# Kernel optimization log

Hardware: AMD Instinct MI355X
Metric: run time of the kernel (lower is better)

The kernel has to match this reference:

```python
import jax, jax.numpy as jnp
import numpy as np

D_IN, D_K, D_V = 1024, 128, 128
B, S = 8, 4096


def setup_inputs() -> dict:
    key = jax.random.key(0)
    kq, kk, kv, kwq, kwk, kwv = jax.random.split(key, 6)
    q = jax.random.normal(kq, (B, S, D_IN), dtype=jnp.float32)
    k = jax.random.normal(kk, (B, S, D_IN), dtype=jnp.float32)
    v = jax.random.normal(kv, (B, S, D_IN), dtype=jnp.float32)
    # nn.Linear(d_in, d_out, bias=None): weight shape [d_out, d_in], y = x @ W^T
    scale = 1.0 / np.sqrt(D_IN)
    Wq = jax.random.uniform(kwq, (D_K, D_IN), jnp.float32, -scale, scale)
    Wk = jax.random.uniform(kwk, (D_K, D_IN), jnp.float32, -scale, scale)
    Wv = jax.random.uniform(kwv, (D_V, D_IN), jnp.float32, -scale, scale)
    return {"q": q, "k": k, "v": v, "Wq": Wq, "Wk": Wk, "Wv": Wv}


def reference(q, k, v, Wq, Wk, Wv):
    # Bias-free projections: [b, s, d_in] @ [d_in, d_k/d_v]
    qh = jnp.einsum('bsd,kd->bsk', q, Wq)
    kh = jnp.einsum('bsd,kd->bsk', k, Wk)
    vh = jnp.einsum('bsd,vd->bsv', v, Wv)
    scores = jnp.einsum('bqk,bsk->bqs', qh, kh) / jnp.sqrt(jnp.float32(D_K))
    attn = jax.nn.softmax(scores, axis=-1)  # [b, s_q, s_kv]
    return jnp.einsum('bqs,bsv->bqv', attn, vh)
```

## Files before the change

### kernel.cpp

```cpp
#include <hip/hip_runtime.h>
#include <hip/hip_bf16.h>
#include <stdint.h>

#define D_IN 1024
#define D_K  128
#define NBATCH 8
#define SEQ  4096
#define MROWS (NBATCH * SEQ)

typedef __attribute__((ext_vector_type(8))) short bf16x8;
typedef __attribute__((ext_vector_type(4))) float f32x4;

__device__ __forceinline__ unsigned short f32_to_bf16(float x) {
    union { float f; uint32_t u; } v; v.f = x;
    uint32_t r = 0x7FFFu + ((v.u >> 16) & 1u);
    return (unsigned short)((v.u + r) >> 16);
}

__device__ __forceinline__ bf16x8 cvt8(float4 lo, float4 hi) {
    bf16x8 r;
    r[0] = (short)f32_to_bf16(lo.x); r[1] = (short)f32_to_bf16(lo.y);
    r[2] = (short)f32_to_bf16(lo.z); r[3] = (short)f32_to_bf16(lo.w);
    r[4] = (short)f32_to_bf16(hi.x); r[5] = (short)f32_to_bf16(hi.y);
    r[6] = (short)f32_to_bf16(hi.z); r[7] = (short)f32_to_bf16(hi.w);
    return r;
}

__device__ __forceinline__ void gload16(const void* src, void* lds) {
    __builtin_amdgcn_global_load_lds(
        (const __attribute__((address_space(1))) void*)src,
        (__attribute__((address_space(3))) void*)lds, 16, 0, 0);
}

__global__ __launch_bounds__(256)
void wconv_kernel(const float* __restrict__ Wq, const float* __restrict__ Wk,
                  const float* __restrict__ Wv, unsigned short* __restrict__ Wt)
{
    const int t  = blockIdx.x * 256 + threadIdx.x;
    const int n  = t & 127;
    const int kc = (t >> 7) & 127;
    const int p  = t >> 14;
    const float* __restrict__ W = (p == 0) ? Wq : (p == 1) ? Wk : Wv;
    const float sc = (p == 0) ? (1.44269504088896f * 0.0883883476483184f) : 1.0f;
    const float4* src = reinterpret_cast<const float4*>(W + (size_t)n * D_IN + kc * 8);
    float4 a = src[0], b = src[1];
    uint4 o;
    o.x = (uint32_t)f32_to_bf16(a.x * sc) | ((uint32_t)f32_to_bf16(a.y * sc) << 16);
    o.y = (uint32_t)f32_to_bf16(a.z * sc) | ((uint32_t)f32_to_bf16(a.w * sc) << 16);
    o.z = (uint32_t)f32_to_bf16(b.x * sc) | ((uint32_t)f32_to_bf16(b.y * sc) << 16);
    o.w = (uint32_t)f32_to_bf16(b.z * sc) | ((uint32_t)f32_to_bf16(b.w * sc) << 16);
    *reinterpret_cast<uint4*>(Wt + (size_t)t * 8) = o;
}

#define RBM 32

__global__ __launch_bounds__(256, 2)
void proj_kernel(const float* __restrict__ Xq, const float* __restrict__ Xk,
                 const float* __restrict__ Xv,
                 const unsigned short* __restrict__ Wt,
                 unsigned short* __restrict__ qh, unsigned short* __restrict__ kh,
                 unsigned short* __restrict__ vhT)
{
    const int p = blockIdx.y;
    const float* __restrict__ X = (p == 0) ? Xq : (p == 1) ? Xk : Xv;
    const unsigned short* __restrict__ Wtp = Wt + (size_t)p * 128 * 128 * 8;

    __shared__ float Asf[2][RBM * 256];

    const int tid  = threadIdx.x;
    const int lane = tid & 63;
    const int w    = tid >> 6;
    const int lrow = lane & 15;
    const int g    = lane >> 4;
    const int wbase = blockIdx.x * RBM;
    const char* __restrict__ Xb = reinterpret_cast<const char*>(X);

    f32x4 acc[2][2];
    #pragma unroll
    for (int mi = 0; mi < 2; ++mi)
        #pragma unroll
        for (int ni = 0; ni < 2; ++ni)
            acc[mi][ni] = (f32x4){0.f, 0.f, 0.f, 0.f};

    const int aswz = (lrow & 7) << 5;
    bf16x8 bb[16];

    #define STAGE_A(buf, kk_)                                                 \
    do {                                                                      \
        _Pragma("unroll")                                                     \
        for (int i = 0; i < 8; ++i) {                                         \
            const int r_ = w * 8 + i;                                         \
            gload16(Xb + (size_t)(wbase + r_) * 4096 + (kk_) * 1024 +         \
                        ((lane * 16) ^ ((r_ & 7) << 5)),                      \
                    reinterpret_cast<char*>(Asf[buf]) + r_ * 1024);           \
        }                                                                     \
    } while (0)

    STAGE_A(0, 0);
    asm volatile("s_waitcnt vmcnt(0)" ::: "memory");
    __syncthreads();

    int buf = 0;
    #pragma unroll
    for (int kk = 0; kk < 4; ++kk) {
        const unsigned short* __restrict__ wbk =
            Wtp + ((size_t)(kk * 32 + g) * 128 + w * 32 + lrow) * 8;
        #pragma unroll
        for (int t = 0; t < 8; ++t)
            #pragma unroll
            for (int ni = 0; ni < 2; ++ni)
                bb[t * 2 + ni] = *reinterpret_cast<const bf16x8*>(
                    wbk + ((size_t)(t * 4) * 128 + ni * 16) * 8);

        if (kk < 3) STAGE_A(buf ^ 1, kk + 1);

        const char* const base = reinterpret_cast<const char*>(Asf[buf]);
        const char* const a0 = base + lrow * 1024;
        const char* const a1 = base + (16 + lrow) * 1024;
        #pragma unroll
        for (int t = 0; t < 8; ++t) {
            const int boff = (t * 128 + g * 32) ^ aswz;
            float4 lo0 = *reinterpret_cast<const float4*>(a0 + boff);
            float4 hi0 = *reinterpret_cast<const float4*>(a0 + boff + 16);
            float4 lo1 = *reinterpret_cast<const float4*>(a1 + boff);
            float4 hi1 = *reinterpret_cast<const float4*>(a1 + boff + 16);
            bf16x8 af0 = cvt8(lo0, hi0);
            bf16x8 af1 = cvt8(lo1, hi1);
            acc[0][0] = __builtin_amdgcn_mfma_f32_16x16x32_bf16(af0, bb[t * 2 + 0], acc[0][0], 0, 0, 0);
            acc[0][1] = __builtin_amdgcn_mfma_f32_16x16x32_bf16(af0, bb[t * 2 + 1], acc[0][1], 0, 0, 0);
            acc[1][0] = __builtin_amdgcn_mfma_f32_16x16x32_bf16(af1, bb[t * 2 + 0], acc[1][0], 0, 0, 0);
            acc[1][1] = __builtin_amdgcn_mfma_f32_16x16x32_bf16(af1, bb[t * 2 + 1], acc[1][1], 0, 0, 0);
        }

        if (kk < 3) {
            __syncthreads();
            buf ^= 1;
        }
    }
    #undef STAGE_A

    if (p < 2) {
        unsigned short* __restrict__ Y = (p == 0) ? qh : kh;
        #pragma unroll
        for (int mi = 0; mi < 2; ++mi) {
            const int rbase = wbase + mi * 16 + g * 4;
            #pragma unroll
            for (int ni = 0; ni < 2; ++ni) {
                const int n = w * 32 + ni * 16 + lrow;
                #pragma unroll
                for (int r = 0; r < 4; ++r)
                    Y[(size_t)(rbase + r) * D_K + n] = f32_to_bf16(acc[mi][ni][r]);
            }
        }
    } else {
        const int b = wbase >> 12;
        #pragma unroll
        for (int mi = 0; mi < 2; ++mi) {
            const int s = (wbase & 4095) + mi * 16 + g * 4;
            #pragma unroll
            for (int ni = 0; ni < 2; ++ni) {
                const int d = w * 32 + ni * 16 + lrow;
                uint2 t;
                t.x = (uint32_t)f32_to_bf16(acc[mi][ni][0]) |
                      ((uint32_t)f32_to_bf16(acc[mi][ni][1]) << 16);
                t.y = (uint32_t)f32_to_bf16(acc[mi][ni][2]) |
                      ((uint32_t)f32_to_bf16(acc[mi][ni][3]) << 16);
                *reinterpret_cast<uint2*>(vhT + ((size_t)(b * D_K + d) << 12) + s) = t;
            }
        }
    }
}

#define KVB 64
#define PSTRIDE 144

__global__ __launch_bounds__(256, 2)
void attn_kernel(const unsigned short* __restrict__ qh,
                 const unsigned short* __restrict__ kh,
                 const unsigned short* __restrict__ vhT,
                 float* __restrict__ out)
{
    __shared__ unsigned short Ks[2][KVB * D_K];
    __shared__ unsigned short Vs[2][D_K * KVB];
    __shared__ char Ps[4][16 * PSTRIDE];

    const int tid  = threadIdx.x;
    const int lane = tid & 63;
    const int wave = tid >> 6;
    const int b    = blockIdx.x & 7;
    const int qt   = blockIdx.x >> 3;
    const int q0   = qt * 64 + wave * 16;
    const int lrow = lane & 15;
    const int g    = lane >> 4;
    const int g4   = g << 2;
    const int lk16 = g * 16;

    const unsigned short* __restrict__ Kb = kh + (size_t)b * SEQ * D_K;
    const unsigned short* __restrict__ Vb = vhT + (size_t)b * D_K * SEQ;
    char* const Pw = Ps[wave];

    const int kr0  = lane >> 4;
    const int kcbp = (lane & 15) * 16;
    const int vr0  = lane >> 3;
    const int vcbp = (lane & 7) * 16;

    #define STAGE(buf, it_)                                                   \
    do {                                                                      \
        const int s0_ = (it_) * KVB;                                          \
        _Pragma("unroll")                                                     \
        for (int j = 0; j < 4; ++j) {                                         \
            const int blk  = wave * 4 + j;                                    \
            const int krow = blk * 4 + kr0;                                   \
            gload16(reinterpret_cast<const char*>(Kb) +                       \
                        (size_t)(s0_ + krow) * 256 +                          \
                        (kcbp ^ ((krow & 7) << 4)),                           \
                    reinterpret_cast<char*>(Ks[buf]) + blk * 1024);           \
            const int vrow = blk * 8 + vr0;                                   \
            gload16(reinterpret_cast<const char*>(Vb) +                       \
                        (size_t)vrow * (SEQ * 2) + (size_t)s0_ * 2 +          \
                        (vcbp ^ ((vrow & 7) << 4)),                           \
                    reinterpret_cast<char*>(Vs[buf]) + blk * 1024);           \
        }                                                                     \
    } while (0)

    bf16x8 qf[4];
    {
        const char* base = reinterpret_cast<const char*>(
            qh + (size_t)(b * SEQ + q0 + lrow) * D_K);
        #pragma unroll
        for (int ks = 0; ks < 4; ++ks)
            qf[ks] = *reinterpret_cast<const bf16x8*>(base + ks * 64 + lk16);
    }

    f32x4 o[8];
    #pragma unroll
    for (int df = 0; df < 8; ++df) o[df] = (f32x4){0.f, 0.f, 0.f, 0.f};
    float lsum = 0.f;

    STAGE(0, 0);
    asm volatile("s_waitcnt vmcnt(0)" ::: "memory");
    __syncthreads();

    int cur = 0;
    for (int it = 0; it < SEQ / KVB; ++it) {
        if (it + 1 < SEQ / KVB) STAGE(cur ^ 1, it + 1);

        f32x4 scT[4];
        #pragma unroll
        for (int sf = 0; sf < 4; ++sf) scT[sf] = (f32x4){0.f, 0.f, 0.f, 0.f};
        #pragma unroll
        for (int ks = 0; ks < 4; ++ks) {
            #pragma unroll
            for (int sf = 0; sf < 4; ++sf) {
                const int row = sf * 16 + lrow;
                bf16x8 kf = *reinterpret_cast<const bf16x8*>(
                    reinterpret_cast<const char*>(Ks[cur]) + row * 256 +
                    ((ks * 64 + lk16) ^ ((row & 7) << 4)));
                scT[sf] = __builtin_amdgcn_mfma_f32_16x16x32_bf16(kf, qf[ks], scT[sf], 0, 0, 0);
            }
        }

        #pragma unroll
        for (int sf = 0; sf < 4; ++sf) {
            float p0 = exp2f(scT[sf][0]);
            float p1 = exp2f(scT[sf][1]);
            float p2 = exp2f(scT[sf][2]);
            float p3 = exp2f(scT[sf][3]);
            lsum += (p0 + p1) + (p2 + p3);
            uint32_t u0, u1;
            asm("v_cvt_pk_bf16_f32 %0, %1, %2" : "=v"(u0) : "v"(p0), "v"(p1));
            asm("v_cvt_pk_bf16_f32 %0, %1, %2" : "=v"(u1) : "v"(p2), "v"(p3));
            uint2 t; t.x = u0; t.y = u1;
            *reinterpret_cast<uint2*>(Pw + lrow * PSTRIDE + (4 * sf + g) * 8) = t;
        }

        #pragma unroll
        for (int ks = 0; ks < 2; ++ks) {
            bf16x8 pf = *reinterpret_cast<const bf16x8*>(
                Pw + lrow * PSTRIDE + ks * 64 + g * 16);
            #pragma unroll
            for (int df = 0; df < 8; ++df) {
                const int vr = df * 16 + lrow;
                bf16x8 vf = *reinterpret_cast<const bf16x8*>(
                    reinterpret_cast<const char*>(Vs[cur]) + vr * 128 +
                    ((ks * 64 + lk16) ^ ((vr & 7) << 4)));
                o[df] = __builtin_amdgcn_mfma_f32_16x16x32_bf16(pf, vf, o[df], 0, 0, 0);
            }
        }

        asm volatile("s_waitcnt vmcnt(0)" ::: "memory");
        __syncthreads();
        cur ^= 1;
    }
    #undef STAGE

    float s = lsum;
    s += __shfl_xor(s, 16);
    s += __shfl_xor(s, 32);
    #pragma unroll
    for (int r = 0; r < 4; ++r) {
        float inv = 1.0f / __shfl(s, g4 + r);
        const int row = q0 + g4 + r;
        float* ob = out + (size_t)(b * SEQ + row) * D_K + lrow;
        #pragma unroll
        for (int df = 0; df < 8; ++df)
            ob[df * 16] = o[df][r] * inv;
    }
}

extern "C" void kernel_launch(void* const* d_in, const int* in_sizes, int n_in,
                              void* d_out, int out_size, void* d_ws, size_t ws_size,
                              hipStream_t stream)
{
    (void)in_sizes; (void)n_in; (void)out_size; (void)ws_size;
    const float* q  = (const float*)d_in[0];
    const float* k  = (const float*)d_in[1];
    const float* v  = (const float*)d_in[2];
    const float* Wq = (const float*)d_in[3];
    const float* Wk = (const float*)d_in[4];
    const float* Wv = (const float*)d_in[5];

    unsigned short* qh  = (unsigned short*)d_ws;
    unsigned short* kh  = qh + (size_t)MROWS * D_K;
    unsigned short* vhT = kh + (size_t)MROWS * D_K;
    unsigned short* Wt  = vhT + (size_t)MROWS * D_K;

    wconv_kernel<<<dim3(192), 256, 0, stream>>>(Wq, Wk, Wv, Wt);
    proj_kernel<<<dim3(MROWS / RBM, 3), 256, 0, stream>>>(q, k, v, Wt, qh, kh, vhT);
    attn_kernel<<<dim3(NBATCH * (SEQ / 64)), 256, 0, stream>>>(qh, kh, vhT, (float*)d_out);
}
```

Measured before the change: 235.0 us.

## Triple-buffer projection A tiles with 128-column stages and manual vmcnt waits

```diff
diff --git a/kernel.cpp b/kernel.cpp
--- a/kernel.cpp
+++ b/kernel.cpp
@@ -54,7 +54,7 @@
 
 #define RBM 32
 
-__global__ __launch_bounds__(256, 2)
+__global__ __launch_bounds__(256, 3)
 void proj_kernel(const float* __restrict__ Xq, const float* __restrict__ Xk,
                  const float* __restrict__ Xv,
                  const unsigned short* __restrict__ Wt,
@@ -65,7 +65,7 @@
     const float* __restrict__ X = (p == 0) ? Xq : (p == 1) ? Xk : Xv;
     const unsigned short* __restrict__ Wtp = Wt + (size_t)p * 128 * 128 * 8;
 
-    __shared__ float Asf[2][RBM * 256];
+    __shared__ char As8[3 * 16384];
 
     const int tid  = threadIdx.x;
     const int lane = tid & 63;
@@ -82,62 +82,69 @@
         for (int ni = 0; ni < 2; ++ni)
             acc[mi][ni] = (f32x4){0.f, 0.f, 0.f, 0.f};
 
-    const int aswz = (lrow & 7) << 5;
-    bf16x8 bb[16];
-
-    #define STAGE_A(buf, kk_)                                                 \
+    const int swzr = ((lrow & 3) << 5) | (((lrow >> 2) & 1) << 4);
+    bf16x8 bb0[8], bb1[8];
+
+    #define STAGE_A8(buf_, e_)                                                \
     do {                                                                      \
         _Pragma("unroll")                                                     \
-        for (int i = 0; i < 8; ++i) {                                         \
-            const int r_ = w * 8 + i;                                         \
-            gload16(Xb + (size_t)(wbase + r_) * 4096 + (kk_) * 1024 +         \
-                        ((lane * 16) ^ ((r_ & 7) << 5)),                      \
-                    reinterpret_cast<char*>(Asf[buf]) + r_ * 1024);           \
+        for (int j = 0; j < 4; ++j) {                                         \
+            const int rr   = w * 8 + 2 * j + (lane >> 5);                     \
+            const int swzb = ((rr & 3) << 5) | (((rr >> 2) & 1) << 4);        \
+            gload16(Xb + (size_t)(wbase + rr) * 4096 + (e_) * 512 +           \
+                        (((lane & 31) * 16) ^ swzb),                          \
+                    As8 + (buf_) * 16384 + (w * 8 + 2 * j) * 512);            \
         }                                                                     \
     } while (0)
 
-    STAGE_A(0, 0);
-    asm volatile("s_waitcnt vmcnt(0)" ::: "memory");
-    __syncthreads();
-
-    int buf = 0;
+    #define LOAD_BB(dst_, e_)                                                 \
+    do {                                                                      \
+        _Pragma("unroll")                                                     \
+        for (int t = 0; t < 4; ++t)                                           \
+            _Pragma("unroll")                                                 \
+            for (int ni = 0; ni < 2; ++ni)                                    \
+                dst_[t * 2 + ni] = *reinterpret_cast<const bf16x8*>(          \
+                    Wtp + ((size_t)(16 * (e_) + 4 * t + g) * 128 +            \
+                           w * 32 + ni * 16 + lrow) * 8);                     \
+    } while (0)
+
+    STAGE_A8(0, 0);
+    STAGE_A8(1, 1);
+    LOAD_BB(bb0, 0);
+
     #pragma unroll
-    for (int kk = 0; kk < 4; ++kk) {
-        const unsigned short* __restrict__ wbk =
-            Wtp + ((size_t)(kk * 32 + g) * 128 + w * 32 + lrow) * 8;
-        #pragma unroll
-        for (int t = 0; t < 8; ++t)
-            #pragma unroll
-            for (int ni = 0; ni < 2; ++ni)
-                bb[t * 2 + ni] = *reinterpret_cast<const bf16x8*>(
-                    wbk + ((size_t)(t * 4) * 128 + ni * 16) * 8);
-
-        if (kk < 3) STAGE_A(buf ^ 1, kk + 1);
-
-        const char* const base = reinterpret_cast<const char*>(Asf[buf]);
-        const char* const a0 = base + lrow * 1024;
-        const char* const a1 = base + (16 + lrow) * 1024;
-        #pragma unroll
-        for (int t = 0; t < 8; ++t) {
-            const int boff = (t * 128 + g * 32) ^ aswz;
-            float4 lo0 = *reinterpret_cast<const float4*>(a0 + boff);
-            float4 hi0 = *reinterpret_cast<const float4*>(a0 + boff + 16);
-            float4 lo1 = *reinterpret_cast<const float4*>(a1 + boff);
-            float4 hi1 = *reinterpret_cast<const float4*>(a1 + boff + 16);
+    for (int e = 0; e < 8; ++e) {
+        __builtin_amdgcn_s_barrier();
+        if (e + 2 < 8) STAGE_A8((e + 2) % 3, e + 2);
+        if (e + 1 < 8) {
+            if ((e & 1) == 0) LOAD_BB(bb1, e + 1);
+            else              LOAD_BB(bb0, e + 1);
+        }
+        if (e <= 5)      asm volatile("s_waitcnt vmcnt(12)" ::: "memory");
+        else if (e == 6) asm volatile("s_waitcnt vmcnt(8)"  ::: "memory");
+        else             asm volatile("s_waitcnt vmcnt(0)"  ::: "memory");
+
+        const char* const bufb = As8 + (e % 3) * 16384;
+        const char* const a0 = bufb + lrow * 512;
+        const char* const a1 = bufb + (16 + lrow) * 512;
+        #pragma unroll
+        for (int t = 0; t < 4; ++t) {
+            const int ob = t * 128 + g * 32;
+            float4 lo0 = *reinterpret_cast<const float4*>(a0 + (ob ^ swzr));
+            float4 hi0 = *reinterpret_cast<const float4*>(a0 + ((ob + 16) ^ swzr));
+            float4 lo1 = *reinterpret_cast<const float4*>(a1 + (ob ^ swzr));
+            float4 hi1 = *reinterpret_cast<const float4*>(a1 + ((ob + 16) ^ swzr));
             bf16x8 af0 = cvt8(lo0, hi0);
             bf16x8 af1 = cvt8(lo1, hi1);
-            acc[0][0] = __builtin_amdgcn_mfma_f32_16x16x32_bf16(af0, bb[t * 2 + 0], acc[0][0], 0, 0, 0);
-            acc[0][1] = __builtin_amdgcn_mfma_f32_16x16x32_bf16(af0, bb[t * 2 + 1], acc[0][1], 0, 0, 0);
-            acc[1][0] = __builtin_amdgcn_mfma_f32_16x16x32_bf16(af1, bb[t * 2 + 0], acc[1][0], 0, 0, 0);
-            acc[1][1] = __builtin_amdgcn_mfma_f32_16x16x32_bf16(af1, bb[t * 2 + 1], acc[1][1], 0, 0, 0);
-        }
-
-        if (kk < 3) {
-            __syncthreads();
-            buf ^= 1;
-        }
-    }
-    #undef STAGE_A
+            const bf16x8* bc = ((e & 1) == 0) ? bb0 : bb1;
+            acc[0][0] = __builtin_amdgcn_mfma_f32_16x16x32_bf16(af0, bc[t * 2 + 0], acc[0][0], 0, 0, 0);
+            acc[0][1] = __builtin_amdgcn_mfma_f32_16x16x32_bf16(af0, bc[t * 2 + 1], acc[0][1], 0, 0, 0);
+            acc[1][0] = __builtin_amdgcn_mfma_f32_16x16x32_bf16(af1, bc[t * 2 + 0], acc[1][0], 0, 0, 0);
+            acc[1][1] = __builtin_amdgcn_mfma_f32_16x16x32_bf16(af1, bc[t * 2 + 1], acc[1][1], 0, 0, 0);
+        }
+    }
+    #undef STAGE_A8
+    #undef LOAD_BB
 
     if (p < 2) {
         unsigned short* __restrict__ Y = (p == 0) ? qh : kh;
```

Measured after the change: 209.2 us. 11.0% less time.
